# Kernel tuning notes

Measured on AMD Instinct MI355X. Metric: run time of the kernel, lower is better.

The kernel has to match this reference:

```python
import jax, jax.numpy as jnp
import numpy as np

B, N, C_IN, C_OUT, CHEB_K, EMB = 32, 2048, 128, 128, 3, 128
LN_EPS = 1e-12


def setup_inputs() -> dict:
    key = jax.random.key(0)
    k0, k1, k2, k3 = jax.random.split(key, 4)
    return {
        "x": jax.random.normal(k0, (B, N, C_IN), dtype=jnp.float32),
        "node_embeddings": jax.random.normal(k1, (N, EMB), dtype=jnp.float32),
        "weights_pool": jax.random.normal(k2, (EMB, CHEB_K, C_IN, C_OUT), dtype=jnp.float32) * 0.02,
        "bias_pool": jax.random.normal(k3, (EMB, C_OUT), dtype=jnp.float32) * 0.02,
        "ln_gamma": jnp.ones((EMB,), dtype=jnp.float32),
        "ln_beta": jnp.zeros((EMB,), dtype=jnp.float32),
    }


def reference(x, node_embeddings, weights_pool, bias_pool, ln_gamma, ln_beta):
    # x: [B, N, C_in]; node_embeddings: [N, D]
    cheb_k = weights_pool.shape[1]
    n = node_embeddings.shape[0]

    # LayerNorm over embed dim (biased variance, eps=1e-12); dropout is eval-mode identity
    mu = jnp.mean(node_embeddings, axis=-1, keepdims=True)
    var = jnp.mean(jnp.square(node_embeddings - mu), axis=-1, keepdims=True)
    e = (node_embeddings - mu) * jax.lax.rsqrt(var + LN_EPS) * ln_gamma + ln_beta

    # Adaptive adjacency: softmax(elu(E E^T)) over last dim (mask=None path)
    supports = jax.nn.softmax(jax.nn.elu(e @ e.T), axis=-1)  # [N, N]

    # Chebyshev polynomial set: T0=I, T1=A, Tk = 2A Tk-1 - Tk-2
    s_list = [jnp.eye(n, dtype=x.dtype), supports]
    for _ in range(2, cheb_k):
        s_list.append(2.0 * supports @ s_list[-1] - s_list[-2])
    S = jnp.stack(s_list, axis=0)  # [K, N, N]

    # Hypernetwork: per-node weights and bias
    weights = jnp.einsum("nd,dkio->nkio", e, weights_pool)  # [N, K, C_in, C_out]
    bias = e @ bias_pool  # [N, C_out]

    # Graph conv: gather neighborhoods per Chebyshev order, then per-node GEMM
    x_g = jnp.einsum("knm,bmc->bnkc", S, x)  # [B, N, K, C_in]
    out = jnp.einsum("bnki,nkio->bno", x_g, weights) + bias  # [B, N, C_out]
    return out
```

## Files before the change

### kernel.cpp

```cpp
#include <hip/hip_runtime.h>

#define DI __device__ __forceinline__

typedef unsigned short u16;
typedef short short8 __attribute__((ext_vector_type(8)));
typedef float f32x4 __attribute__((ext_vector_type(4)));
typedef u16 u16x4 __attribute__((ext_vector_type(4)));

#define NN 2048
#define CC 128
#define BB 32
#define DD 128
#define OO 128
#define KI 384
#define JJ 49152

DI u16 f2bf(float f) {
  union { float f; unsigned u; } v; v.f = f;
  return (u16)((v.u + 0x7fffu + ((v.u >> 16) & 1u)) >> 16);
}
DI float bf2f(u16 h) {
  union { unsigned u; float f; } v; v.u = ((unsigned)h) << 16;
  return v.f;
}

typedef __attribute__((address_space(3))) unsigned int lds_u32;
typedef __attribute__((address_space(1))) unsigned int glob_u32;

DI void gl16(const void* g, void* l) {
  __builtin_amdgcn_global_load_lds((const glob_u32*)g, (lds_u32*)l, 16, 0, 0);
}

__global__ __launch_bounds__(128)
void k_ln(const float* __restrict__ emb, const float* __restrict__ gam,
          const float* __restrict__ bet, float* __restrict__ e,
          u16* __restrict__ ehi, u16* __restrict__ elo) {
  __shared__ float s2[2], q2[2];
  const int n = blockIdx.x, t = threadIdx.x;
  const float v = emb[(size_t)n * DD + t];
  float s = v;
  #pragma unroll
  for (int off = 32; off; off >>= 1) s += __shfl_down(s, off);
  if ((t & 63) == 0) s2[t >> 6] = s;
  __syncthreads();
  const float mu = (s2[0] + s2[1]) * (1.f / 128.f);
  const float dv = v - mu;
  float q = dv * dv;
  #pragma unroll
  for (int off = 32; off; off >>= 1) q += __shfl_down(q, off);
  if ((t & 63) == 0) q2[t >> 6] = q;
  __syncthreads();
  const float var = (q2[0] + q2[1]) * (1.f / 128.f);
  const float ev = dv * rsqrtf(var + 1e-12f) * gam[t] + bet[t];
  e[(size_t)n * DD + t] = ev;
  const u16 hi = f2bf(ev);
  ehi[(size_t)n * DD + t] = hi;
  elo[(size_t)n * DD + t] = f2bf(ev - bf2f(hi));
}

__global__ __launch_bounds__(256, 2)
void k_zg(const u16* __restrict__ ehi, const u16* __restrict__ elo, float* __restrict__ Z) {
  __shared__ char smem[32768];
  const int t = threadIdx.x;
  const int w = t >> 6, l = t & 63;
  const int l15 = l & 15, kg = l >> 4;
  const int wr = (w >> 1) * 64, wc = (w & 1) * 64;
  const int row0 = blockIdx.x * 128, col0 = blockIdx.y * 128;

  f32x4 acc[4][4];
  #pragma unroll
  for (int i = 0; i < 4; ++i)
    #pragma unroll
    for (int j = 0; j < 4; ++j) { f32x4 z = {0.f, 0.f, 0.f, 0.f}; acc[i][j] = z; }

  const int ra = t >> 3, sa = t & 7;
  #pragma unroll 1
  for (int it = 0; it < 6; ++it) {
    const int term = it >> 1;
    const int k0 = (it & 1) * 64;
    const u16* As = (term == 2) ? elo : ehi;
    const u16* Bs = (term == 1) ? elo : ehi;
    __syncthreads();
    #pragma unroll
    for (int i = 0; i < 4; ++i) {
      const int r = i * 32 + ra;
      const int ss = sa ^ (r & 7);
      gl16(As + (size_t)(row0 + r) * DD + k0 + ss * 8, smem + i * 4096 + t * 16);
      gl16(Bs + (size_t)(col0 + r) * DD + k0 + ss * 8, smem + 16384 + i * 4096 + t * 16);
    }
    __syncthreads();
    short8 af[2][4], bfv[2][4];
    #pragma unroll
    for (int mt = 0; mt < 4; ++mt) {
      const int row = wr + mt * 16 + l15;
      #pragma unroll
      for (int ks = 0; ks < 2; ++ks) {
        const int sl = (ks * 4 + kg) ^ (row & 7);
        af[ks][mt] = *(const short8*)(smem + row * 128 + sl * 16);
      }
    }
    #pragma unroll
    for (int nt = 0; nt < 4; ++nt) {
      const int row = wc + nt * 16 + l15;
      #pragma unroll
      for (int ks = 0; ks < 2; ++ks) {
        const int sl = (ks * 4 + kg) ^ (row & 7);
        bfv[ks][nt] = *(const short8*)(smem + 16384 + row * 128 + sl * 16);
      }
    }
    #pragma unroll
    for (int ks = 0; ks < 2; ++ks)
      #pragma unroll
      for (int mt = 0; mt < 4; ++mt)
        #pragma unroll
        for (int nt = 0; nt < 4; ++nt)
          acc[mt][nt] = __builtin_amdgcn_mfma_f32_16x16x32_bf16(af[ks][mt], bfv[ks][nt], acc[mt][nt], 0, 0, 0);
  }
  #pragma unroll
  for (int mt = 0; mt < 4; ++mt) {
    const int n_ = row0 + wr + mt * 16 + kg * 4;
    #pragma unroll
    for (int nt = 0; nt < 4; ++nt) {
      const int m_ = col0 + wc + nt * 16 + l15;
      #pragma unroll
      for (int r = 0; r < 4; ++r) {
        const float v = acc[mt][nt][r];
        Z[(size_t)(n_ + r) * NN + m_] = (v > 0.f) ? v : expm1f(v);
      }
    }
  }
}

__global__ __launch_bounds__(256)
void k_sm(const float* __restrict__ Z, u16* __restrict__ Abf) {
  __shared__ float red[4];
  const int n = blockIdx.x, t = threadIdx.x, w = t >> 6;
  const float* zr = Z + (size_t)n * NN + t * 8;
  float4 v0 = *(const float4*)(zr);
  float4 v1 = *(const float4*)(zr + 4);
  float z[8] = {v0.x, v0.y, v0.z, v0.w, v1.x, v1.y, v1.z, v1.w};
  float mx = z[0];
  #pragma unroll
  for (int i = 1; i < 8; ++i) mx = fmaxf(mx, z[i]);
  #pragma unroll
  for (int off = 32; off; off >>= 1) mx = fmaxf(mx, __shfl_xor(mx, off));
  if ((t & 63) == 0) red[w] = mx;
  __syncthreads();
  mx = fmaxf(fmaxf(red[0], red[1]), fmaxf(red[2], red[3]));
  __syncthreads();
  float sm = 0.f;
  #pragma unroll
  for (int i = 0; i < 8; ++i) { z[i] = expf(z[i] - mx); sm += z[i]; }
  #pragma unroll
  for (int off = 32; off; off >>= 1) sm += __shfl_xor(sm, off);
  if ((t & 63) == 0) red[w] = sm;
  __syncthreads();
  const float inv = 1.f / (red[0] + red[1] + red[2] + red[3]);
  short8 pk;
  #pragma unroll
  for (int i = 0; i < 8; ++i) pk[i] = (short)f2bf(z[i] * inv);
  *(short8*)(Abf + (size_t)n * NN + t * 8) = pk;
}

__global__ __launch_bounds__(256)
void k_tc(const float* __restrict__ x, u16* __restrict__ xt, u16* __restrict__ xbf) {
  __shared__ float ld[64 * 68];
  const int t = threadIdx.x;
  const int m0 = blockIdx.x * 64, c0 = blockIdx.y * 64, b = blockIdx.z;
  const float* xb = x + (size_t)b * NN * CC;
  u16* xfb = xbf + (size_t)b * NN * CC;
  #pragma unroll
  for (int i = 0; i < 4; ++i) {
    const int m = i * 16 + (t >> 4), c4 = (t & 15) * 4;
    const float4 v = *(const float4*)&xb[(size_t)(m0 + m) * CC + c0 + c4];
    *(float4*)&ld[m * 68 + c4] = v;
    u16x4 cv = { f2bf(v.x), f2bf(v.y), f2bf(v.z), f2bf(v.w) };
    *(u16x4*)&xfb[(size_t)(m0 + m) * CC + c0 + c4] = cv;
  }
  __syncthreads();
  u16* xtb = xt + (size_t)b * CC * NN;
  #pragma unroll
  for (int i = 0; i < 4; ++i) {
    const int c = i * 16 + (t >> 4), m4 = (t & 15) * 4;
    u16x4 v = { f2bf(ld[(m4 + 0) * 68 + c]), f2bf(ld[(m4 + 1) * 68 + c]),
                f2bf(ld[(m4 + 2) * 68 + c]), f2bf(ld[(m4 + 3) * 68 + c]) };
    *(u16x4*)&xtb[(size_t)(c0 + c) * NN + m0 + m4] = v;
  }
}

__global__ __launch_bounds__(256)
void k_wpt(const float* __restrict__ wp, u16* __restrict__ wpt) {
  __shared__ float ld[64 * 68];
  const int t = threadIdx.x;
  const int d0 = blockIdx.x * 64, o0 = blockIdx.y * 64, ki = blockIdx.z;
  #pragma unroll
  for (int i = 0; i < 4; ++i) {
    const int d = i * 16 + (t >> 4), o4 = (t & 15) * 4;
    *(float4*)&ld[d * 68 + o4] = *(const float4*)&wp[((size_t)(d0 + d) * KI + ki) * OO + o0 + o4];
  }
  __syncthreads();
  #pragma unroll
  for (int i = 0; i < 4; ++i) {
    const int o = i * 16 + (t >> 4), d4 = (t & 15) * 4;
    u16x4 v = { f2bf(ld[(d4 + 0) * 68 + o]), f2bf(ld[(d4 + 1) * 68 + o]),
                f2bf(ld[(d4 + 2) * 68 + o]), f2bf(ld[(d4 + 3) * 68 + o]) };
    *(u16x4*)&wpt[((size_t)(o0 + o) * KI + ki) * DD + d0 + d4] = v;
  }
}

__global__ __launch_bounds__(128)
void k_bias(const float* __restrict__ e, const float* __restrict__ bp, float* __restrict__ bias) {
  const int n = blockIdx.x, o = threadIdx.x;
  const float* er = e + (size_t)n * DD;
  float acc = 0.f;
  for (int d = 0; d < 128; ++d) acc = fmaf(er[d], bp[(size_t)d * OO + o], acc);
  bias[(size_t)n * OO + o] = acc;
}

template<int MODE>
__global__ __launch_bounds__(256, 2)
void gemm_bf16(const u16* __restrict__ Ab, int lda,
               const u16* __restrict__ Bb, int ldb, int ksteps,
               u16* __restrict__ out0, u16* __restrict__ out1,
               const u16* __restrict__ xaux) {
  __shared__ char smem[34816];
  const int t = threadIdx.x;
  const int w = t >> 6, l = t & 63;
  const int l15 = l & 15, kg = l >> 4;
  const int wr = (w >> 1) * 64, wc = (w & 1) * 64;

  const u16 *Abase, *Bbase;
  int row0 = 0, col0 = 0, b = 0;
  if constexpr (MODE == 0 || MODE == 1) {
    const int lin = blockIdx.x + (int)gridDim.x * blockIdx.y;
    const int xcd = lin & 7, pos = lin >> 3;
    const int tile = xcd * 2 + (pos & 1);
    b = pos >> 1;
    if constexpr (MODE == 0) {
      row0 = tile * 128;
      Abase = Ab + (size_t)row0 * lda;
      Bbase = Bb + (size_t)b * CC * NN;
    } else {
      col0 = tile * 128;
      Abase = Ab + (size_t)b * CC * NN;
      Bbase = Bb + (size_t)col0 * NN;
    }
  } else {
    row0 = blockIdx.x * 128; col0 = blockIdx.y * 128;
    Abase = Ab + (size_t)row0 * 128;
    Bbase = Bb + (size_t)col0 * 128;
  }

  f32x4 acc[4][4];
  #pragma unroll
  for (int i = 0; i < 4; ++i)
    #pragma unroll
    for (int j = 0; j < 4; ++j) { f32x4 z = {0.f, 0.f, 0.f, 0.f}; acc[i][j] = z; }

  const int ra = t >> 3, sa = t & 7;
  for (int kt = 0; kt < ksteps; ++kt) {
    const int k0 = kt * 64;
    __syncthreads();
    #pragma unroll
    for (int i = 0; i < 4; ++i) {
      const int r = i * 32 + ra;
      const int ss = sa ^ (r & 7);
      gl16(Abase + (size_t)r * lda + k0 + ss * 8, smem + i * 4096 + t * 16);
    }
    #pragma unroll
    for (int i = 0; i < 4; ++i) {
      const int r = i * 32 + ra;
      const int ss = sa ^ (r & 7);
      gl16(Bbase + (size_t)r * ldb + k0 + ss * 8, smem + 16384 + i * 4096 + t * 16);
    }
    __syncthreads();
    short8 af[2][4], bfv[2][4];
    #pragma unroll
    for (int mt = 0; mt < 4; ++mt) {
      const int row = wr + mt * 16 + l15;
      #pragma unroll
      for (int ks = 0; ks < 2; ++ks) {
        const int sl = (ks * 4 + kg) ^ (row & 7);
        af[ks][mt] = *(const short8*)(smem + row * 128 + sl * 16);
      }
    }
    #pragma unroll
    for (int nt = 0; nt < 4; ++nt) {
      const int row = wc + nt * 16 + l15;
      #pragma unroll
      for (int ks = 0; ks < 2; ++ks) {
        const int sl = (ks * 4 + kg) ^ (row & 7);
        bfv[ks][nt] = *(const short8*)(smem + 16384 + row * 128 + sl * 16);
      }
    }
    #pragma unroll
    for (int ks = 0; ks < 2; ++ks)
      #pragma unroll
      for (int mt = 0; mt < 4; ++mt)
        #pragma unroll
        for (int nt = 0; nt < 4; ++nt)
          acc[mt][nt] = __builtin_amdgcn_mfma_f32_16x16x32_bf16(af[ks][mt], bfv[ks][nt], acc[mt][nt], 0, 0, 0);
  }

  if constexpr (MODE == 0) {
    u16* y1t = out0 + (size_t)b * CC * NN;
    #pragma unroll
    for (int mt = 0; mt < 4; ++mt) {
      const int n_ = row0 + wr + mt * 16 + kg * 4;
      #pragma unroll
      for (int nt = 0; nt < 4; ++nt) {
        const int c_ = wc + nt * 16 + l15;
        u16x4 v = { f2bf(acc[mt][nt][0]), f2bf(acc[mt][nt][1]),
                    f2bf(acc[mt][nt][2]), f2bf(acc[mt][nt][3]) };
        *(u16x4*)(y1t + (size_t)c_ * NN + n_) = v;
      }
    }
    __syncthreads();
    u16* L = (u16*)smem;
    #pragma unroll
    for (int mt = 0; mt < 4; ++mt) {
      const int nl = wr + mt * 16 + kg * 4;
      #pragma unroll
      for (int nt = 0; nt < 4; ++nt) {
        const int c_ = wc + nt * 16 + l15;
        #pragma unroll
        for (int r = 0; r < 4; ++r) L[(nl + r) * 136 + c_] = f2bf(acc[mt][nt][r]);
      }
    }
    __syncthreads();
    u16* y1o = out1 + (size_t)b * NN * CC;
    const int nl2 = t >> 1, ch = (t & 1) * 64;
    #pragma unroll
    for (int q = 0; q < 8; ++q) {
      short8 vv = *(const short8*)(L + nl2 * 136 + ch + q * 8);
      *(short8*)(y1o + (size_t)(row0 + nl2) * CC + ch + q * 8) = vv;
    }
  } else if constexpr (MODE == 1) {
    const u16* xb = xaux + (size_t)b * NN * CC;
    u16* y2b = out0 + (size_t)b * NN * CC;
    #pragma unroll
    for (int mt = 0; mt < 4; ++mt) {
      const int c_ = wr + mt * 16 + kg * 4;
      #pragma unroll
      for (int nt = 0; nt < 4; ++nt) {
        const int n_ = col0 + wc + nt * 16 + l15;
        const u16x4 xv = *(const u16x4*)(xb + (size_t)n_ * CC + c_);
        u16x4 v = { f2bf(2.f * acc[mt][nt][0] - bf2f(xv[0])),
                    f2bf(2.f * acc[mt][nt][1] - bf2f(xv[1])),
                    f2bf(2.f * acc[mt][nt][2] - bf2f(xv[2])),
                    f2bf(2.f * acc[mt][nt][3] - bf2f(xv[3])) };
        *(u16x4*)(y2b + (size_t)n_ * CC + c_) = v;
      }
    }
  } else {
    u16* wtb = out0 + (size_t)(row0 >> 7) * ((size_t)gridDim.y << 14);
    #pragma unroll
    for (int mt = 0; mt < 4; ++mt) {
      const int jl = wr + mt * 16 + kg * 4;
      #pragma unroll
      for (int nt = 0; nt < 4; ++nt) {
        const int nl = col0 + wc + nt * 16 + l15;
        u16x4 v = { f2bf(acc[mt][nt][0]), f2bf(acc[mt][nt][1]),
                    f2bf(acc[mt][nt][2]), f2bf(acc[mt][nt][3]) };
        *(u16x4*)(wtb + (size_t)nl * 128 + jl) = v;
      }
    }
  }
}

__global__ __launch_bounds__(256, 4)
void stage_b(const u16* __restrict__ xbf, const u16* __restrict__ y1,
             const u16* __restrict__ y2, const u16* __restrict__ Wt,
             const float* __restrict__ bias, float* __restrict__ out, int nbase) {
  const int t = threadIdx.x, w = t >> 6, l = t & 63;
  const int l15 = l & 15, kg = l >> 4;
  const int n = nbase + blockIdx.x;
  const size_t pstride = (size_t)gridDim.x << 7;
  const u16* Wn = Wt + (size_t)blockIdx.x * 128;
  f32x4 acc[2][2];
  {
    f32x4 z = {0.f, 0.f, 0.f, 0.f};
    acc[0][0] = z; acc[0][1] = z; acc[1][0] = z; acc[1][1] = z;
  }
  #pragma unroll
  for (int ch2 = 0; ch2 < 3; ++ch2) {
    const u16* src = (ch2 == 0) ? xbf : (ch2 == 1) ? y1 : y2;
    #pragma unroll
    for (int ks = 0; ks < 4; ++ks) {
      short8 af[2];
      #pragma unroll
      for (int mt = 0; mt < 2; ++mt) {
        const int bb2 = mt * 16 + l15;
        af[mt] = *(const short8*)(src + ((size_t)bb2 * NN + n) * CC + ks * 32 + kg * 8);
      }
      #pragma unroll
      for (int ot = 0; ot < 2; ++ot) {
        const int o = w * 32 + ot * 16 + l15;
        short8 bv = *(const short8*)(Wn + (size_t)(3 * o + ch2) * pstride + ks * 32 + kg * 8);
        acc[0][ot] = __builtin_amdgcn_mfma_f32_16x16x32_bf16(af[0], bv, acc[0][ot], 0, 0, 0);
        acc[1][ot] = __builtin_amdgcn_mfma_f32_16x16x32_bf16(af[1], bv, acc[1][ot], 0, 0, 0);
      }
    }
  }
  #pragma unroll
  for (int ot = 0; ot < 2; ++ot) {
    const int o = w * 32 + ot * 16 + l15;
    const float bs = bias[(size_t)n * OO + o];
    #pragma unroll
    for (int mt = 0; mt < 2; ++mt)
      #pragma unroll
      for (int r = 0; r < 4; ++r) {
        const int bb2 = mt * 16 + kg * 4 + r;
        out[((size_t)bb2 * NN + n) * OO + o] = acc[mt][ot][r] + bs;
      }
  }
}

extern "C" void kernel_launch(void* const* d_in, const int* in_sizes, int n_in,
                              void* d_out, int out_size, void* d_ws, size_t ws_size,
                              hipStream_t stream) {
  (void)in_sizes; (void)n_in; (void)out_size;
  const float* x   = (const float*)d_in[0];
  const float* emb = (const float*)d_in[1];
  const float* wp  = (const float*)d_in[2];
  const float* bp  = (const float*)d_in[3];
  const float* gam = (const float*)d_in[4];
  const float* bet = (const float*)d_in[5];
  float* out = (float*)d_out;
  char* ws = (char*)d_ws;

  size_t off = 0;
  auto alloc = [&](size_t bytes) -> void* {
    void* p = (void*)(ws + off);
    off += (bytes + 511) & ~(size_t)511;
    return p;
  };
  float* e    = (float*)alloc((size_t)NN * DD * 4);
  u16*   ehi  = (u16*)  alloc((size_t)NN * DD * 2);
  u16*   elo  = (u16*)  alloc((size_t)NN * DD * 2);
  float* bias = (float*)alloc((size_t)NN * OO * 4);
  u16*   Abf  = (u16*)  alloc((size_t)NN * NN * 2);
  u16*   xt   = (u16*)  alloc((size_t)BB * CC * NN * 2);
  u16*   xbf  = (u16*)  alloc((size_t)BB * NN * CC * 2);
  u16*   y1t  = (u16*)  alloc((size_t)BB * CC * NN * 2);
  u16*   y1   = (u16*)  alloc((size_t)BB * NN * CC * 2);
  u16*   y2   = (u16*)  alloc((size_t)BB * NN * CC * 2);
  u16*   wpt  = (u16*)  alloc((size_t)JJ * DD * 2);
  const size_t rem = (ws_size > off) ? (ws_size - off) : 0;
  int chunk = 1024;
  while (chunk > 128 && (size_t)chunk * JJ * 2 > rem) chunk >>= 1;
  size_t wt_bytes = (size_t)chunk * JJ * 2;
  const size_t z_bytes = (size_t)NN * NN * 4;
  u16* wt = (u16*)alloc(wt_bytes > z_bytes ? wt_bytes : z_bytes);
  float* Z = (float*)wt;

  k_ln<<<NN, 128, 0, stream>>>(emb, gam, bet, e, ehi, elo);
  k_zg<<<dim3(16, 16), 256, 0, stream>>>(ehi, elo, Z);
  k_sm<<<NN, 256, 0, stream>>>(Z, Abf);
  k_tc<<<dim3(NN / 64, CC / 64, BB), 256, 0, stream>>>(x, xt, xbf);
  k_wpt<<<dim3(2, 2, KI), 256, 0, stream>>>(wp, wpt);
  k_bias<<<NN, 128, 0, stream>>>(e, bp, bias);

  gemm_bf16<0><<<dim3(16, 32), 256, 0, stream>>>(Abf, NN, xt, NN, 32, y1t, y1, nullptr);
  gemm_bf16<1><<<dim3(16, 32), 256, 0, stream>>>(y1t, NN, Abf, NN, 32, y2, nullptr, xbf);

  for (int nb = 0; nb < NN; nb += chunk) {
    gemm_bf16<2><<<dim3(JJ / 128, chunk / 128), 256, 0, stream>>>(
        wpt, DD, ehi + (size_t)nb * DD, DD, 2, wt, nullptr, nullptr);
    stage_b<<<chunk, 256, 0, stream>>>(xbf, y1, y2, wt, bias, out, nb);
  }
}
```

Measured before the change: 355.1 us.

## Co-schedule propagation GEMMs with hypernetwork weight GEMMs in merged launches

```diff
diff --git a/kernel.cpp b/kernel.cpp
--- a/kernel.cpp
+++ b/kernel.cpp
@@ -217,13 +217,28 @@
   bias[(size_t)n * OO + o] = acc;
 }
 
-template<int MODE>
+struct GJob {
+  const u16* A; const u16* B;
+  u16* out0; u16* out1;
+  const u16* xaux;
+  int lda, ldb, ksteps, mode, gx, gy;
+};
+
 __global__ __launch_bounds__(256, 2)
-void gemm_bf16(const u16* __restrict__ Ab, int lda,
-               const u16* __restrict__ Bb, int ldb, int ksteps,
-               u16* __restrict__ out0, u16* __restrict__ out1,
-               const u16* __restrict__ xaux) {
+void gemm_rt(GJob ja, GJob jb, int nA, int ilv) {
   __shared__ char smem[34816];
+  const int bid = blockIdx.x;
+  bool first;
+  int lb;
+  if (ilv > 1) {
+    const int q = bid / ilv, r = bid - q * ilv;
+    first = (r == 0);
+    lb = first ? q : q * (ilv - 1) + (r - 1);
+  } else {
+    first = bid < nA;
+    lb = first ? bid : bid - nA;
+  }
+  const GJob j = first ? ja : jb;
   const int t = threadIdx.x;
   const int w = t >> 6, l = t & 63;
   const int l15 = l & 15, kg = l >> 4;
@@ -231,47 +246,47 @@
 
   const u16 *Abase, *Bbase;
   int row0 = 0, col0 = 0, b = 0;
-  if constexpr (MODE == 0 || MODE == 1) {
-    const int lin = blockIdx.x + (int)gridDim.x * blockIdx.y;
-    const int xcd = lin & 7, pos = lin >> 3;
+  if (j.mode <= 1) {
+    const int xcd = lb & 7, pos = lb >> 3;
     const int tile = xcd * 2 + (pos & 1);
     b = pos >> 1;
-    if constexpr (MODE == 0) {
+    if (j.mode == 0) {
       row0 = tile * 128;
-      Abase = Ab + (size_t)row0 * lda;
-      Bbase = Bb + (size_t)b * CC * NN;
+      Abase = j.A + (size_t)row0 * j.lda;
+      Bbase = j.B + (size_t)b * CC * NN;
     } else {
       col0 = tile * 128;
-      Abase = Ab + (size_t)b * CC * NN;
-      Bbase = Bb + (size_t)col0 * NN;
+      Abase = j.A + (size_t)b * CC * NN;
+      Bbase = j.B + (size_t)col0 * NN;
     }
   } else {
-    row0 = blockIdx.x * 128; col0 = blockIdx.y * 128;
-    Abase = Ab + (size_t)row0 * 128;
-    Bbase = Bb + (size_t)col0 * 128;
+    const int jx = lb % j.gx, jy = lb / j.gx;
+    row0 = jx * 128; col0 = jy * 128;
+    Abase = j.A + (size_t)row0 * 128;
+    Bbase = j.B + (size_t)col0 * 128;
   }
 
   f32x4 acc[4][4];
   #pragma unroll
   for (int i = 0; i < 4; ++i)
     #pragma unroll
-    for (int j = 0; j < 4; ++j) { f32x4 z = {0.f, 0.f, 0.f, 0.f}; acc[i][j] = z; }
+    for (int jq = 0; jq < 4; ++jq) { f32x4 z = {0.f, 0.f, 0.f, 0.f}; acc[i][jq] = z; }
 
   const int ra = t >> 3, sa = t & 7;
-  for (int kt = 0; kt < ksteps; ++kt) {
+  for (int kt = 0; kt < j.ksteps; ++kt) {
     const int k0 = kt * 64;
     __syncthreads();
     #pragma unroll
     for (int i = 0; i < 4; ++i) {
       const int r = i * 32 + ra;
       const int ss = sa ^ (r & 7);
-      gl16(Abase + (size_t)r * lda + k0 + ss * 8, smem + i * 4096 + t * 16);
+      gl16(Abase + (size_t)r * j.lda + k0 + ss * 8, smem + i * 4096 + t * 16);
     }
     #pragma unroll
     for (int i = 0; i < 4; ++i) {
       const int r = i * 32 + ra;
       const int ss = sa ^ (r & 7);
-      gl16(Bbase + (size_t)r * ldb + k0 + ss * 8, smem + 16384 + i * 4096 + t * 16);
+      gl16(Bbase + (size_t)r * j.ldb + k0 + ss * 8, smem + 16384 + i * 4096 + t * 16);
     }
     __syncthreads();
     short8 af[2][4], bfv[2][4];
@@ -302,8 +317,8 @@
           acc[mt][nt] = __builtin_amdgcn_mfma_f32_16x16x32_bf16(af[ks][mt], bfv[ks][nt], acc[mt][nt], 0, 0, 0);
   }
 
-  if constexpr (MODE == 0) {
-    u16* y1t = out0 + (size_t)b * CC * NN;
+  if (j.mode == 0) {
+    u16* y1t = j.out0 + (size_t)b * CC * NN;
     #pragma unroll
     for (int mt = 0; mt < 4; ++mt) {
       const int n_ = row0 + wr + mt * 16 + kg * 4;
@@ -328,16 +343,16 @@
       }
     }
     __syncthreads();
-    u16* y1o = out1 + (size_t)b * NN * CC;
+    u16* y1o = j.out1 + (size_t)b * NN * CC;
     const int nl2 = t >> 1, ch = (t & 1) * 64;
     #pragma unroll
     for (int q = 0; q < 8; ++q) {
       short8 vv = *(const short8*)(L + nl2 * 136 + ch + q * 8);
       *(short8*)(y1o + (size_t)(row0 + nl2) * CC + ch + q * 8) = vv;
     }
-  } else if constexpr (MODE == 1) {
-    const u16* xb = xaux + (size_t)b * NN * CC;
-    u16* y2b = out0 + (size_t)b * NN * CC;
+  } else if (j.mode == 1) {
+    const u16* xb = j.xaux + (size_t)b * NN * CC;
+    u16* y2b = j.out0 + (size_t)b * NN * CC;
     #pragma unroll
     for (int mt = 0; mt < 4; ++mt) {
       const int c_ = wr + mt * 16 + kg * 4;
@@ -353,7 +368,7 @@
       }
     }
   } else {
-    u16* wtb = out0 + (size_t)(row0 >> 7) * ((size_t)gridDim.y << 14);
+    u16* wtb = j.out0 + (size_t)(row0 >> 7) * ((size_t)j.gy << 14);
     #pragma unroll
     for (int mt = 0; mt < 4; ++mt) {
       const int jl = wr + mt * 16 + kg * 4;
@@ -370,13 +385,16 @@
 
 __global__ __launch_bounds__(256, 4)
 void stage_b(const u16* __restrict__ xbf, const u16* __restrict__ y1,
-             const u16* __restrict__ y2, const u16* __restrict__ Wt,
+             const u16* __restrict__ y2, const u16* __restrict__ wtA,
+             const u16* __restrict__ wtB, int npb,
              const float* __restrict__ bias, float* __restrict__ out, int nbase) {
   const int t = threadIdx.x, w = t >> 6, l = t & 63;
   const int l15 = l & 15, kg = l >> 4;
-  const int n = nbase + blockIdx.x;
-  const size_t pstride = (size_t)gridDim.x << 7;
-  const u16* Wn = Wt + (size_t)blockIdx.x * 128;
+  const int bidx = blockIdx.x;
+  const int n = nbase + bidx;
+  const bool lo = bidx < npb;
+  const size_t pstride = (size_t)npb << 7;
+  const u16* Wn = (lo ? wtA : wtB) + (size_t)(lo ? bidx : bidx - npb) * 128;
   f32x4 acc[2][2];
   {
     f32x4 z = {0.f, 0.f, 0.f, 0.f};
@@ -447,26 +465,44 @@
   u16*   y2   = (u16*)  alloc((size_t)BB * NN * CC * 2);
   u16*   wpt  = (u16*)  alloc((size_t)JJ * DD * 2);
   const size_t rem = (ws_size > off) ? (ws_size - off) : 0;
-  int chunk = 1024;
-  while (chunk > 128 && (size_t)chunk * JJ * 2 > rem) chunk >>= 1;
-  size_t wt_bytes = (size_t)chunk * JJ * 2;
-  const size_t z_bytes = (size_t)NN * NN * 4;
-  u16* wt = (u16*)alloc(wt_bytes > z_bytes ? wt_bytes : z_bytes);
-  float* Z = (float*)wt;
-
-  k_ln<<<NN, 128, 0, stream>>>(emb, gam, bet, e, ehi, elo);
-  k_zg<<<dim3(16, 16), 256, 0, stream>>>(ehi, elo, Z);
-  k_sm<<<NN, 256, 0, stream>>>(Z, Abf);
-  k_tc<<<dim3(NN / 64, CC / 64, BB), 256, 0, stream>>>(x, xt, xbf);
-  k_wpt<<<dim3(2, 2, KI), 256, 0, stream>>>(wp, wpt);
-  k_bias<<<NN, 128, 0, stream>>>(e, bp, bias);
-
-  gemm_bf16<0><<<dim3(16, 32), 256, 0, stream>>>(Abf, NN, xt, NN, 32, y1t, y1, nullptr);
-  gemm_bf16<1><<<dim3(16, 32), 256, 0, stream>>>(y1t, NN, Abf, NN, 32, y2, nullptr, xbf);
-
-  for (int nb = 0; nb < NN; nb += chunk) {
-    gemm_bf16<2><<<dim3(JJ / 128, chunk / 128), 256, 0, stream>>>(
-        wpt, DD, ehi + (size_t)nb * DD, DD, 2, wt, nullptr, nullptr);
-    stage_b<<<chunk, 256, 0, stream>>>(xbf, y1, y2, wt, bias, out, nb);
-  }
-}
+  const size_t half_wt = (size_t)1024 * JJ * 2;
+  const bool planA = rem >= 2 * half_wt + 1024;
+
+  auto prep = [&](float* Z) {
+    k_ln<<<NN, 128, 0, stream>>>(emb, gam, bet, e, ehi, elo);
+    k_zg<<<dim3(16, 16), 256, 0, stream>>>(ehi, elo, Z);
+    k_sm<<<NN, 256, 0, stream>>>(Z, Abf);
+    k_tc<<<dim3(NN / 64, CC / 64, BB), 256, 0, stream>>>(x, xt, xbf);
+    k_wpt<<<dim3(2, 2, KI), 256, 0, stream>>>(wp, wpt);
+    k_bias<<<NN, 128, 0, stream>>>(e, bp, bias);
+  };
+
+  GJob jg0 = { Abf, xt,  y1t, y1,      nullptr, NN, NN, 32, 0, 0, 0 };
+  GJob jg1 = { y1t, Abf, y2,  nullptr, xbf,     NN, NN, 32, 1, 0, 0 };
+
+  if (planA) {
+    u16* wt0 = (u16*)alloc(half_wt);
+    u16* wt1 = (u16*)alloc(half_wt);
+    prep((float*)wt0);
+    GJob jg2a = { wpt, ehi,                       wt0, nullptr, nullptr, DD, DD, 2, 2, 384, 8 };
+    GJob jg2b = { wpt, ehi + (size_t)1024 * DD,   wt1, nullptr, nullptr, DD, DD, 2, 2, 384, 8 };
+    gemm_rt<<<512 * 7, 256, 0, stream>>>(jg0, jg2a, 512, 7);
+    gemm_rt<<<512 * 7, 256, 0, stream>>>(jg1, jg2b, 512, 7);
+    stage_b<<<2048, 256, 0, stream>>>(xbf, y1, y2, wt0, wt1, 1024, bias, out, 0);
+  } else {
+    int chunk = 1024;
+    while (chunk > 128 && (size_t)chunk * JJ * 2 > rem) chunk >>= 1;
+    size_t wt_bytes = (size_t)chunk * JJ * 2;
+    const size_t z_bytes = (size_t)NN * NN * 4;
+    u16* wt = (u16*)alloc(wt_bytes > z_bytes ? wt_bytes : z_bytes);
+    prep((float*)wt);
+    gemm_rt<<<512, 256, 0, stream>>>(jg0, jg0, 512, 0);
+    gemm_rt<<<512, 256, 0, stream>>>(jg1, jg1, 512, 0);
+    const int gy = chunk / 128;
+    for (int nb = 0; nb < NN; nb += chunk) {
+      GJob jg2 = { wpt, ehi + (size_t)nb * DD, wt, nullptr, nullptr, DD, DD, 2, 2, 384, gy };
+      gemm_rt<<<384 * gy, 256, 0, stream>>>(jg2, jg2, 384 * gy, 0);
+      stage_b<<<chunk, 256, 0, stream>>>(xbf, y1, y2, wt, wt, chunk, bias, out, nb);
+    }
+  }
+}
```

Result: no change. 360.1 us (+1.4%).
